# Kernel optimization log

Measured on AMD Instinct MI355X. Metric: run time of the kernel, lower is better.

## Reference

```python
import jax, jax.numpy as jnp
import numpy as np

B, C, H, W = 16384, 1, 2048, 1
HID = 5


def setup_inputs() -> dict:
    key = jax.random.key(0)
    kx, kl, k1, k2, k3, k4 = jax.random.split(key, 6)
    x = jax.random.normal(kx, (B, C, H, W), dtype=jnp.float32)
    # random ragged lengths in [1, H]; zero out padded tail so the module's
    # (x != 0).any(dim=2) mask recovers exactly these lengths
    lengths = jax.random.randint(kl, (B,), 1, H + 1)
    t_idx = jnp.arange(H)
    valid = (t_idx[None, :] < lengths[:, None])  # [B, H]
    x = x * valid[:, None, :, None].astype(jnp.float32)
    s = 1.0 / np.sqrt(HID)
    W_ih = jax.random.uniform(k1, (4 * HID, 1), minval=-s, maxval=s, dtype=jnp.float32)
    W_hh = jax.random.uniform(k2, (4 * HID, HID), minval=-s, maxval=s, dtype=jnp.float32)
    b_ih = jax.random.uniform(k3, (4 * HID,), minval=-s, maxval=s, dtype=jnp.float32)
    b_hh = jax.random.uniform(k4, (4 * HID,), minval=-s, maxval=s, dtype=jnp.float32)
    return {"x": x, "W_ih": W_ih, "W_hh": W_hh, "b_ih": b_ih, "b_hh": b_hh}


def reference(x, W_ih, W_hh, b_ih, b_hh):
    b, c, h, w = x.shape
    feats = c * w  # == 1 (LSTM input_size)
    xr = x.reshape(b, h, feats)  # [B, T, 1]
    mask = jnp.any(xr != 0, axis=2)  # [B, T]
    lengths = mask.sum(axis=1).astype(jnp.int32)  # [B]

    bias = b_ih + b_hh  # [4H]
    # precompute input projection for all timesteps: [B, T, 4H]
    x_proj = jnp.einsum('btf,gf->btg', xr, W_ih) + bias
    xs = jnp.moveaxis(x_proj, 1, 0)  # [T, B, 4H]

    h0 = jnp.zeros((b, HID), dtype=x.dtype)
    c0 = jnp.zeros((b, HID), dtype=x.dtype)

    def step(carry, inp):
        hp, cp = carry
        xg, t = inp
        gates = xg + hp @ W_hh.T  # [B, 4H]
        i, f, g, o = jnp.split(gates, 4, axis=1)
        i = jax.nn.sigmoid(i)
        f = jax.nn.sigmoid(f)
        g = jnp.tanh(g)
        o = jax.nn.sigmoid(o)
        cn = f * cp + i * g
        hn = o * jnp.tanh(cn)
        # packed semantics: only advance state while t < length (per sample)
        upd = (t < lengths)[:, None]
        hn = jnp.where(upd, hn, hp)
        cn = jnp.where(upd, cn, cp)
        return (hn, cn), None

    (hT, cT), _ = jax.lax.scan(step, (h0, c0), (xs, jnp.arange(h)))
    return hT[None]  # [1, B, HID] matching torch h shape
```

## Files before the change

kernel.cpp:

```cpp
#include <hip/hip_runtime.h>

#define Bn    16384
#define Tn    2048
#define HIDn  5
#define NBINS 2048

typedef float v2f __attribute__((ext_vector_type(2)));

static __device__ __forceinline__ float rcp_fast(float v) {
    return __builtin_amdgcn_rcpf(v);
}
static __device__ __forceinline__ float med3(float x, float lo, float hi) {
    return __builtin_amdgcn_fmed3f(x, lo, hi);
}

template <int K>
static __device__ __forceinline__ float bcast8(float v) {
    return __int_as_float(
        __builtin_amdgcn_ds_swizzle(__float_as_int(v), (K << 5) | 0x18));
}

__global__ void zero_kernel(int* __restrict__ gbins) {
    gbins[blockIdx.x * 256 + threadIdx.x] = 0;
}

__global__ __launch_bounds__(256) void len_kernel(const float* __restrict__ x,
                                                  int* __restrict__ lengths,
                                                  int* __restrict__ gbins) {
    const int gtid = blockIdx.x * 256 + threadIdx.x;
    const int row  = gtid >> 6;
    const int lane = threadIdx.x & 63;
    const float4* r = reinterpret_cast<const float4*>(x + (size_t)row * Tn);
    int cnt = 0;
    #pragma unroll
    for (int i = 0; i < Tn / 4 / 64; ++i) {
        float4 v = r[i * 64 + lane];
        cnt += (v.x != 0.0f) + (v.y != 0.0f) + (v.z != 0.0f) + (v.w != 0.0f);
    }
    #pragma unroll
    for (int off = 32; off > 0; off >>= 1) cnt += __shfl_xor(cnt, off, 64);
    if (lane == 0) {
        lengths[row] = cnt;
        const int d = max(0, min(NBINS - 1, NBINS - cnt));
        atomicAdd(&gbins[d], 1);
    }
}

__global__ __launch_bounds__(1024) void sort_kernel(const int* __restrict__ lengths,
                                                    const int* __restrict__ gbins,
                                                    int* __restrict__ perm) {
    __shared__ int bins[NBINS];
    __shared__ int bsum[1024];
    const int tid = threadIdx.x;
    bins[tid]        = gbins[tid];
    bins[tid + 1024] = gbins[tid + 1024];
    __syncthreads();
    const int a0 = bins[2 * tid], a1 = bins[2 * tid + 1];
    const int s = a0 + a1;
    bsum[tid] = s;
    __syncthreads();
    int acc = s;
    for (int off = 1; off < 1024; off <<= 1) {
        int v = (tid >= off) ? bsum[tid - off] : 0;
        __syncthreads();
        acc += v;
        bsum[tid] = acc;
        __syncthreads();
    }
    const int excl = acc - s;
    bins[2 * tid]     = excl;
    bins[2 * tid + 1] = excl + a0;
    __syncthreads();
    for (int i = tid; i < Bn; i += 1024) {
        int d = NBINS - lengths[i];
        d = max(0, min(NBINS - 1, d));
        const int p = atomicAdd(&bins[d], 1);
        perm[p] = i;
    }
}

__global__ __launch_bounds__(256, 2) void lstm_kernel(const float* __restrict__ x,
                                                      const float* __restrict__ Wih,
                                                      const float* __restrict__ Whh,
                                                      const float* __restrict__ bih,
                                                      const float* __restrict__ bhh,
                                                      const int* __restrict__ lengths,
                                                      const int* __restrict__ perm,
                                                      float* __restrict__ out) {
    const int gtid = blockIdx.x * 256 + threadIdx.x;
    const int grp  = gtid >> 3;
    const int lsub = threadIdx.x & 7;
    const int k    = min(lsub, 4);

    const int b   = perm[grp];
    const int len = lengths[b];

    v2f wihA, wihB, bA, bB, whhA[HIDn], whhB[HIDn];
    {
        const int gi = k, gf = 5 + k, gg = 10 + k, go = 15 + k;
        wihA = (v2f){ Wih[gi] * 0.5f, Wih[gf] * 0.5f };
        wihB = (v2f){ Wih[gg],        Wih[go] * 0.5f };
        bA   = (v2f){ (bih[gi] + bhh[gi]) * 0.5f, (bih[gf] + bhh[gf]) * 0.5f };
        bB   = (v2f){ (bih[gg] + bhh[gg]),        (bih[go] + bhh[go]) * 0.5f };
        #pragma unroll
        for (int kk = 0; kk < HIDn; ++kk) {
            whhA[kk] = (v2f){ Whh[gi * HIDn + kk] * 0.5f, Whh[gf * HIDn + kk] * 0.5f };
            whhB[kk] = (v2f){ Whh[gg * HIDn + kk],        Whh[go * HIDn + kk] * 0.5f };
        }
    }

    const float* xrow = x + (size_t)b * Tn;
    float h0 = 0, h1 = 0, h2 = 0, h3 = 0, h4 = 0;
    float hq = 0, c = 0;

    float4 xq = *reinterpret_cast<const float4*>(xrow);
    for (int t = 0; __any(t < len); t += 4) {
        const float4 xn = *reinterpret_cast<const float4*>(xrow + min(t + 4, Tn - 4));
        const float xs[4] = { xq.x, xq.y, xq.z, xq.w };
        #pragma unroll
        for (int s = 0; s < 4; ++s) {
            const float xv = xs[s];
            v2f pA = xv * wihA + bA;
            v2f pB = xv * wihB + bB;
            pA = h0 * whhA[0] + pA;  pB = h0 * whhB[0] + pB;
            pA = h1 * whhA[1] + pA;  pB = h1 * whhB[1] + pB;
            pA = h2 * whhA[2] + pA;  pB = h2 * whhB[2] + pB;
            pA = h3 * whhA[3] + pA;  pB = h3 * whhB[3] + pB;
            pA = h4 * whhA[4] + pA;  pB = h4 * whhB[4] + pB;
            v2f tA, tB;
            tA.x = med3(pA.x, -4.0f, 4.0f);  tA.y = med3(pA.y, -4.0f, 4.0f);
            tB.x = med3(pB.x, -4.0f, 4.0f);  tB.y = med3(pB.y, -4.0f, 4.0f);
            const v2f zA = tA * tA, zB = tB * tB;
            const v2f nA = (zA * 21.0f + 1260.0f) * zA + 10395.0f;
            const v2f nB = (zB * 21.0f + 1260.0f) * zB + 10395.0f;
            const v2f dA = ((zA + 210.0f) * zA + 4725.0f) * zA + 10395.0f;
            const v2f dB = ((zB + 210.0f) * zB + 4725.0f) * zB + 10395.0f;
            const float rA = rcp_fast(dA.x * dA.y);
            const float rB = rcp_fast(dB.x * dB.y);
            const v2f pnA = tA * nA, pnB = tB * nB;
            const float ti = (pnA.x * dA.y) * rA;
            const float tf = (pnA.y * dA.x) * rA;
            const float tg = (pnB.x * dB.y) * rB;
            const float to = (pnB.y * dB.x) * rB;
            const float gi_ = fmaf(ti, 0.5f, 0.5f);
            const float gf_ = fmaf(tf, 0.5f, 0.5f);
            const float oo  = fmaf(to, 0.5f, 0.5f);

            const float cn = fmaf(gf_, c, gi_ * tg);

            const float tc = med3(cn, -4.0f, 4.0f);
            const float zc = tc * tc;
            const float nc = fmaf(zc, fmaf(zc, 21.0f, 1260.0f), 10395.0f);
            const float dc = fmaf(zc, fmaf(zc, zc + 210.0f, 4725.0f), 10395.0f);
            const float hn = (tc * nc) * (oo * rcp_fast(dc));

            const bool upd = (t + s) < len;
            c  = upd ? cn : c;
            hq = upd ? hn : hq;

            h0 = bcast8<0>(hq);
            h1 = bcast8<1>(hq);
            h2 = bcast8<2>(hq);
            h3 = bcast8<3>(hq);
            h4 = bcast8<4>(hq);
        }
        xq = xn;
    }

    if (lsub < HIDn) out[(size_t)b * HIDn + lsub] = hq;
}

extern "C" void kernel_launch(void* const* d_in, const int* in_sizes, int n_in,
                              void* d_out, int out_size, void* d_ws, size_t ws_size,
                              hipStream_t stream) {
    const float* x   = (const float*)d_in[0];
    const float* Wih = (const float*)d_in[1];
    const float* Whh = (const float*)d_in[2];
    const float* bih = (const float*)d_in[3];
    const float* bhh = (const float*)d_in[4];
    float* out = (float*)d_out;

    int* lengths = (int*)d_ws;
    int* perm    = lengths + Bn;
    int* gbins   = perm + Bn;

    zero_kernel<<<NBINS / 256, 256, 0, stream>>>(gbins);
    len_kernel<<<Bn / 4, 256, 0, stream>>>(x, lengths, gbins);
    sort_kernel<<<1, 1024, 0, stream>>>(lengths, gbins, perm);
    lstm_kernel<<<Bn * 8 / 256, 256, 0, stream>>>(x, Wih, Whh, bih, bhh,
                                                  lengths, perm, out);
}
```

Before: 572.9 us.

## Interleave two independent LSTM sequences per 8-lane group for ILP

Each 8-lane group now advances two sorted-adjacent sequences in lockstep, interleaving their per-step gate math and swizzle broadcasts so the two independent dependency chains can hide each other's latency. The grid is halved and the launch bound drops to one block per SIMD to allow the extra registers. The gate scaling is also partly packed into v2f ops. The costs are fewer resident waves and running each pair to the longer of the two lengths.

```diff
diff --git a/kernel.cpp b/kernel.cpp
--- a/kernel.cpp
+++ b/kernel.cpp
@@ -79,7 +79,51 @@
     }
 }
 
-__global__ __launch_bounds__(256, 2) void lstm_kernel(const float* __restrict__ x,
+static __device__ __forceinline__ void lstm_step(
+    float xv, bool upd,
+    v2f wihA, v2f wihB, v2f bA, v2f bB,
+    const v2f* __restrict__ whhA, const v2f* __restrict__ whhB,
+    float h0, float h1, float h2, float h3, float h4,
+    float& hq, float& c)
+{
+    v2f pA = xv * wihA + bA;
+    v2f pB = xv * wihB + bB;
+    pA = h0 * whhA[0] + pA;  pB = h0 * whhB[0] + pB;
+    pA = h1 * whhA[1] + pA;  pB = h1 * whhB[1] + pB;
+    pA = h2 * whhA[2] + pA;  pB = h2 * whhB[2] + pB;
+    pA = h3 * whhA[3] + pA;  pB = h3 * whhB[3] + pB;
+    pA = h4 * whhA[4] + pA;  pB = h4 * whhB[4] + pB;
+    v2f tA, tB;
+    tA.x = med3(pA.x, -4.0f, 4.0f);  tA.y = med3(pA.y, -4.0f, 4.0f);
+    tB.x = med3(pB.x, -4.0f, 4.0f);  tB.y = med3(pB.y, -4.0f, 4.0f);
+    const v2f zA = tA * tA, zB = tB * tB;
+    const v2f nA = (zA * 21.0f + 1260.0f) * zA + 10395.0f;
+    const v2f nB = (zB * 21.0f + 1260.0f) * zB + 10395.0f;
+    const v2f dA = ((zA + 210.0f) * zA + 4725.0f) * zA + 10395.0f;
+    const v2f dB = ((zB + 210.0f) * zB + 4725.0f) * zB + 10395.0f;
+    const float rA = rcp_fast(dA.x * dA.y);
+    const float rB = rcp_fast(dB.x * dB.y);
+    const v2f pnA = tA * nA, pnB = tB * nB;
+    const v2f dAs = {dA.y, dA.x};
+    const v2f dBs = {dB.y, dB.x};
+    const v2f tAv = (pnA * dAs) * rA;
+    const v2f tBv = (pnB * dBs) * rB;
+    const v2f sA = tAv * 0.5f + 0.5f;
+    const v2f sB = tBv * (v2f){1.0f, 0.5f} + (v2f){0.0f, 0.5f};
+
+    const float cn = fmaf(sA.y, c, sA.x * sB.x);
+
+    const float tc = med3(cn, -4.0f, 4.0f);
+    const float zc = tc * tc;
+    const float nc = fmaf(zc, fmaf(zc, 21.0f, 1260.0f), 10395.0f);
+    const float dc = fmaf(zc, fmaf(zc, zc + 210.0f, 4725.0f), 10395.0f);
+    const float hn = (tc * nc) * (sB.y * rcp_fast(dc));
+
+    c  = upd ? cn : c;
+    hq = upd ? hn : hq;
+}
+
+__global__ __launch_bounds__(256, 1) void lstm_kernel(const float* __restrict__ x,
                                                       const float* __restrict__ Wih,
                                                       const float* __restrict__ Whh,
                                                       const float* __restrict__ bih,
@@ -92,8 +136,11 @@
     const int lsub = threadIdx.x & 7;
     const int k    = min(lsub, 4);
 
-    const int b   = perm[grp];
-    const int len = lengths[b];
+    const int ra = perm[2 * grp];
+    const int rb = perm[2 * grp + 1];
+    const int lenA = lengths[ra];
+    const int lenB = lengths[rb];
+    const int lenM = max(lenA, lenB);
 
     v2f wihA, wihB, bA, bB, whhA[HIDn], whhB[HIDn];
     {
@@ -109,65 +156,47 @@
         }
     }
 
-    const float* xrow = x + (size_t)b * Tn;
-    float h0 = 0, h1 = 0, h2 = 0, h3 = 0, h4 = 0;
-    float hq = 0, c = 0;
-
-    float4 xq = *reinterpret_cast<const float4*>(xrow);
-    for (int t = 0; __any(t < len); t += 4) {
-        const float4 xn = *reinterpret_cast<const float4*>(xrow + min(t + 4, Tn - 4));
-        const float xs[4] = { xq.x, xq.y, xq.z, xq.w };
+    const float* xrA = x + (size_t)ra * Tn;
+    const float* xrB = x + (size_t)rb * Tn;
+
+    float hA0 = 0, hA1 = 0, hA2 = 0, hA3 = 0, hA4 = 0, hqA = 0, cA = 0;
+    float hB0 = 0, hB1 = 0, hB2 = 0, hB3 = 0, hB4 = 0, hqB = 0, cB = 0;
+
+    float4 xqA = *reinterpret_cast<const float4*>(xrA);
+    float4 xqB = *reinterpret_cast<const float4*>(xrB);
+
+    for (int t = 0; __any(t < lenM); t += 4) {
+        const int tn = min(t + 4, Tn - 4);
+        const float4 xnA = *reinterpret_cast<const float4*>(xrA + tn);
+        const float4 xnB = *reinterpret_cast<const float4*>(xrB + tn);
+        const float xsA[4] = { xqA.x, xqA.y, xqA.z, xqA.w };
+        const float xsB[4] = { xqB.x, xqB.y, xqB.z, xqB.w };
         #pragma unroll
         for (int s = 0; s < 4; ++s) {
-            const float xv = xs[s];
-            v2f pA = xv * wihA + bA;
-            v2f pB = xv * wihB + bB;
-            pA = h0 * whhA[0] + pA;  pB = h0 * whhB[0] + pB;
-            pA = h1 * whhA[1] + pA;  pB = h1 * whhB[1] + pB;
-            pA = h2 * whhA[2] + pA;  pB = h2 * whhB[2] + pB;
-            pA = h3 * whhA[3] + pA;  pB = h3 * whhB[3] + pB;
-            pA = h4 * whhA[4] + pA;  pB = h4 * whhB[4] + pB;
-            v2f tA, tB;
-            tA.x = med3(pA.x, -4.0f, 4.0f);  tA.y = med3(pA.y, -4.0f, 4.0f);
-            tB.x = med3(pB.x, -4.0f, 4.0f);  tB.y = med3(pB.y, -4.0f, 4.0f);
-            const v2f zA = tA * tA, zB = tB * tB;
-            const v2f nA = (zA * 21.0f + 1260.0f) * zA + 10395.0f;
-            const v2f nB = (zB * 21.0f + 1260.0f) * zB + 10395.0f;
-            const v2f dA = ((zA + 210.0f) * zA + 4725.0f) * zA + 10395.0f;
-            const v2f dB = ((zB + 210.0f) * zB + 4725.0f) * zB + 10395.0f;
-            const float rA = rcp_fast(dA.x * dA.y);
-            const float rB = rcp_fast(dB.x * dB.y);
-            const v2f pnA = tA * nA, pnB = tB * nB;
-            const float ti = (pnA.x * dA.y) * rA;
-            const float tf = (pnA.y * dA.x) * rA;
-            const float tg = (pnB.x * dB.y) * rB;
-            const float to = (pnB.y * dB.x) * rB;
-            const float gi_ = fmaf(ti, 0.5f, 0.5f);
-            const float gf_ = fmaf(tf, 0.5f, 0.5f);
-            const float oo  = fmaf(to, 0.5f, 0.5f);
-
-            const float cn = fmaf(gf_, c, gi_ * tg);
-
-            const float tc = med3(cn, -4.0f, 4.0f);
-            const float zc = tc * tc;
-            const float nc = fmaf(zc, fmaf(zc, 21.0f, 1260.0f), 10395.0f);
-            const float dc = fmaf(zc, fmaf(zc, zc + 210.0f, 4725.0f), 10395.0f);
-            const float hn = (tc * nc) * (oo * rcp_fast(dc));
-
-            const bool upd = (t + s) < len;
-            c  = upd ? cn : c;
-            hq = upd ? hn : hq;
-
-            h0 = bcast8<0>(hq);
-            h1 = bcast8<1>(hq);
-            h2 = bcast8<2>(hq);
-            h3 = bcast8<3>(hq);
-            h4 = bcast8<4>(hq);
+            lstm_step(xsA[s], (t + s) < lenA, wihA, wihB, bA, bB, whhA, whhB,
+                      hA0, hA1, hA2, hA3, hA4, hqA, cA);
+            hA0 = bcast8<0>(hqA);
+            hA1 = bcast8<1>(hqA);
+            hA2 = bcast8<2>(hqA);
+            hA3 = bcast8<3>(hqA);
+            hA4 = bcast8<4>(hqA);
+
+            lstm_step(xsB[s], (t + s) < lenB, wihA, wihB, bA, bB, whhA, whhB,
+                      hB0, hB1, hB2, hB3, hB4, hqB, cB);
+            hB0 = bcast8<0>(hqB);
+            hB1 = bcast8<1>(hqB);
+            hB2 = bcast8<2>(hqB);
+            hB3 = bcast8<3>(hqB);
+            hB4 = bcast8<4>(hqB);
         }
-        xq = xn;
-    }
-
-    if (lsub < HIDn) out[(size_t)b * HIDn + lsub] = hq;
+        xqA = xnA;
+        xqB = xnB;
+    }
+
+    if (lsub < HIDn) {
+        out[(size_t)ra * HIDn + lsub] = hqA;
+        out[(size_t)rb * HIDn + lsub] = hqB;
+    }
 }
 
 extern "C" void kernel_launch(void* const* d_in, const int* in_sizes, int n_in,
@@ -187,6 +216,6 @@
     zero_kernel<<<NBINS / 256, 256, 0, stream>>>(gbins);
     len_kernel<<<Bn / 4, 256, 0, stream>>>(x, lengths, gbins);
     sort_kernel<<<1, 1024, 0, stream>>>(lengths, gbins, perm);
-    lstm_kernel<<<Bn * 8 / 256, 256, 0, stream>>>(x, Wih, Whh, bih, bhh,
+    lstm_kernel<<<Bn * 8 / 512, 256, 0, stream>>>(x, Wih, Whh, bih, bhh,
                                                   lengths, perm, out);
 }
```

Result: slower. 809.0 us (+41.2%).

## Map each LSTM sample to four lanes with DPP quad broadcast of hidden state

Applied to the files above, without the earlier changes.

Each sample now uses 4 lanes instead of 8. Every lane computes two hidden units: its own unit k, plus unit 4 computed redundantly by all four lanes. The hidden-state exchange moves from ds_swizzle to quad DPP moves, which do not go through the LDS path, and unit 4 is read locally. This halves the thread count and removes the 3 idle lanes per group. In exchange each lane does roughly double the arithmetic, uses more registers, and the occupancy hint drops to 1.

```diff
diff --git a/kernel.cpp b/kernel.cpp
--- a/kernel.cpp
+++ b/kernel.cpp
@@ -15,9 +15,10 @@
 }
 
 template <int K>
-static __device__ __forceinline__ float bcast8(float v) {
+static __device__ __forceinline__ float qbcast(float v) {
+    constexpr int ctrl = K | (K << 2) | (K << 4) | (K << 6);
     return __int_as_float(
-        __builtin_amdgcn_ds_swizzle(__float_as_int(v), (K << 5) | 0x18));
+        __builtin_amdgcn_mov_dpp(__float_as_int(v), ctrl, 0xF, 0xF, true));
 }
 
 __global__ void zero_kernel(int* __restrict__ gbins) {
@@ -79,7 +80,7 @@
     }
 }
 
-__global__ __launch_bounds__(256, 2) void lstm_kernel(const float* __restrict__ x,
+__global__ __launch_bounds__(256, 1) void lstm_kernel(const float* __restrict__ x,
                                                       const float* __restrict__ Wih,
                                                       const float* __restrict__ Whh,
                                                       const float* __restrict__ bih,
@@ -88,30 +89,37 @@
                                                       const int* __restrict__ perm,
                                                       float* __restrict__ out) {
     const int gtid = blockIdx.x * 256 + threadIdx.x;
-    const int grp  = gtid >> 3;
-    const int lsub = threadIdx.x & 7;
-    const int k    = min(lsub, 4);
+    const int grp  = gtid >> 2;
+    const int k    = threadIdx.x & 3;
 
     const int b   = perm[grp];
     const int len = lengths[b];
 
-    v2f wihA, wihB, bA, bB, whhA[HIDn], whhB[HIDn];
-    {
-        const int gi = k, gf = 5 + k, gg = 10 + k, go = 15 + k;
-        wihA = (v2f){ Wih[gi] * 0.5f, Wih[gf] * 0.5f };
-        wihB = (v2f){ Wih[gg],        Wih[go] * 0.5f };
-        bA   = (v2f){ (bih[gi] + bhh[gi]) * 0.5f, (bih[gf] + bhh[gf]) * 0.5f };
-        bB   = (v2f){ (bih[gg] + bhh[gg]),        (bih[go] + bhh[go]) * 0.5f };
-        #pragma unroll
-        for (int kk = 0; kk < HIDn; ++kk) {
-            whhA[kk] = (v2f){ Whh[gi * HIDn + kk] * 0.5f, Whh[gf * HIDn + kk] * 0.5f };
-            whhB[kk] = (v2f){ Whh[gg * HIDn + kk],        Whh[go * HIDn + kk] * 0.5f };
-        }
+    const int ri0 = k,      ri1 = 4;
+    const int rf0 = 5 + k,  rf1 = 9;
+    const int rg0 = 10 + k, rg1 = 14;
+    const int ro0 = 15 + k, ro1 = 19;
+
+    const v2f wI = { Wih[ri0] * 0.5f, Wih[ri1] * 0.5f };
+    const v2f wF = { Wih[rf0] * 0.5f, Wih[rf1] * 0.5f };
+    const v2f wG = { Wih[rg0],        Wih[rg1]        };
+    const v2f wO = { Wih[ro0] * 0.5f, Wih[ro1] * 0.5f };
+    const v2f bI = { (bih[ri0] + bhh[ri0]) * 0.5f, (bih[ri1] + bhh[ri1]) * 0.5f };
+    const v2f bF = { (bih[rf0] + bhh[rf0]) * 0.5f, (bih[rf1] + bhh[rf1]) * 0.5f };
+    const v2f bG = { (bih[rg0] + bhh[rg0]),        (bih[rg1] + bhh[rg1])        };
+    const v2f bO = { (bih[ro0] + bhh[ro0]) * 0.5f, (bih[ro1] + bhh[ro1]) * 0.5f };
+    v2f hI[HIDn], hF[HIDn], hG[HIDn], hO[HIDn];
+    #pragma unroll
+    for (int j = 0; j < HIDn; ++j) {
+        hI[j] = (v2f){ Whh[ri0 * HIDn + j] * 0.5f, Whh[ri1 * HIDn + j] * 0.5f };
+        hF[j] = (v2f){ Whh[rf0 * HIDn + j] * 0.5f, Whh[rf1 * HIDn + j] * 0.5f };
+        hG[j] = (v2f){ Whh[rg0 * HIDn + j],        Whh[rg1 * HIDn + j]        };
+        hO[j] = (v2f){ Whh[ro0 * HIDn + j] * 0.5f, Whh[ro1 * HIDn + j] * 0.5f };
     }
 
     const float* xrow = x + (size_t)b * Tn;
+    v2f hq = { 0.0f, 0.0f }, c = { 0.0f, 0.0f };
     float h0 = 0, h1 = 0, h2 = 0, h3 = 0, h4 = 0;
-    float hq = 0, c = 0;
 
     float4 xq = *reinterpret_cast<const float4*>(xrow);
     for (int t = 0; __any(t < len); t += 4) {
@@ -120,54 +128,66 @@
         #pragma unroll
         for (int s = 0; s < 4; ++s) {
             const float xv = xs[s];
-            v2f pA = xv * wihA + bA;
-            v2f pB = xv * wihB + bB;
-            pA = h0 * whhA[0] + pA;  pB = h0 * whhB[0] + pB;
-            pA = h1 * whhA[1] + pA;  pB = h1 * whhB[1] + pB;
-            pA = h2 * whhA[2] + pA;  pB = h2 * whhB[2] + pB;
-            pA = h3 * whhA[3] + pA;  pB = h3 * whhB[3] + pB;
-            pA = h4 * whhA[4] + pA;  pB = h4 * whhB[4] + pB;
-            v2f tA, tB;
-            tA.x = med3(pA.x, -4.0f, 4.0f);  tA.y = med3(pA.y, -4.0f, 4.0f);
-            tB.x = med3(pB.x, -4.0f, 4.0f);  tB.y = med3(pB.y, -4.0f, 4.0f);
-            const v2f zA = tA * tA, zB = tB * tB;
-            const v2f nA = (zA * 21.0f + 1260.0f) * zA + 10395.0f;
-            const v2f nB = (zB * 21.0f + 1260.0f) * zB + 10395.0f;
-            const v2f dA = ((zA + 210.0f) * zA + 4725.0f) * zA + 10395.0f;
-            const v2f dB = ((zB + 210.0f) * zB + 4725.0f) * zB + 10395.0f;
-            const float rA = rcp_fast(dA.x * dA.y);
-            const float rB = rcp_fast(dB.x * dB.y);
-            const v2f pnA = tA * nA, pnB = tB * nB;
-            const float ti = (pnA.x * dA.y) * rA;
-            const float tf = (pnA.y * dA.x) * rA;
-            const float tg = (pnB.x * dB.y) * rB;
-            const float to = (pnB.y * dB.x) * rB;
-            const float gi_ = fmaf(ti, 0.5f, 0.5f);
-            const float gf_ = fmaf(tf, 0.5f, 0.5f);
-            const float oo  = fmaf(to, 0.5f, 0.5f);
-
-            const float cn = fmaf(gf_, c, gi_ * tg);
-
-            const float tc = med3(cn, -4.0f, 4.0f);
-            const float zc = tc * tc;
-            const float nc = fmaf(zc, fmaf(zc, 21.0f, 1260.0f), 10395.0f);
-            const float dc = fmaf(zc, fmaf(zc, zc + 210.0f, 4725.0f), 10395.0f);
-            const float hn = (tc * nc) * (oo * rcp_fast(dc));
+            v2f pI = xv * wI + bI;
+            v2f pF = xv * wF + bF;
+            v2f pG = xv * wG + bG;
+            v2f pO = xv * wO + bO;
+            pI = h0 * hI[0] + pI; pF = h0 * hF[0] + pF; pG = h0 * hG[0] + pG; pO = h0 * hO[0] + pO;
+            pI = h1 * hI[1] + pI; pF = h1 * hF[1] + pF; pG = h1 * hG[1] + pG; pO = h1 * hO[1] + pO;
+            pI = h2 * hI[2] + pI; pF = h2 * hF[2] + pF; pG = h2 * hG[2] + pG; pO = h2 * hO[2] + pO;
+            pI = h3 * hI[3] + pI; pF = h3 * hF[3] + pF; pG = h3 * hG[3] + pG; pO = h3 * hO[3] + pO;
+            pI = h4 * hI[4] + pI; pF = h4 * hF[4] + pF; pG = h4 * hG[4] + pG; pO = h4 * hO[4] + pO;
+            v2f tI, tF, tG, tO;
+            tI.x = med3(pI.x, -4.0f, 4.0f);  tI.y = med3(pI.y, -4.0f, 4.0f);
+            tF.x = med3(pF.x, -4.0f, 4.0f);  tF.y = med3(pF.y, -4.0f, 4.0f);
+            tG.x = med3(pG.x, -4.0f, 4.0f);  tG.y = med3(pG.y, -4.0f, 4.0f);
+            tO.x = med3(pO.x, -4.0f, 4.0f);  tO.y = med3(pO.y, -4.0f, 4.0f);
+            const v2f zI = tI * tI, zF = tF * tF, zG = tG * tG, zO = tO * tO;
+            const v2f nI = (zI * 21.0f + 1260.0f) * zI + 10395.0f;
+            const v2f nF = (zF * 21.0f + 1260.0f) * zF + 10395.0f;
+            const v2f nG = (zG * 21.0f + 1260.0f) * zG + 10395.0f;
+            const v2f nO = (zO * 21.0f + 1260.0f) * zO + 10395.0f;
+            const v2f dI = ((zI + 210.0f) * zI + 4725.0f) * zI + 10395.0f;
+            const v2f dF = ((zF + 210.0f) * zF + 4725.0f) * zF + 10395.0f;
+            const v2f dG = ((zG + 210.0f) * zG + 4725.0f) * zG + 10395.0f;
+            const v2f dO = ((zO + 210.0f) * zO + 4725.0f) * zO + 10395.0f;
+            const v2f prIF = dI * dF;
+            const v2f prGO = dG * dO;
+            const v2f rIF = { rcp_fast(prIF.x), rcp_fast(prIF.y) };
+            const v2f rGO = { rcp_fast(prGO.x), rcp_fast(prGO.y) };
+            const v2f thI = ((tI * nI) * dF) * rIF;
+            const v2f thF = ((tF * nF) * dI) * rIF;
+            const v2f thG = ((tG * nG) * dO) * rGO;
+            const v2f thO = ((tO * nO) * dG) * rGO;
+            const v2f sI = thI * 0.5f + 0.5f;
+            const v2f sF = thF * 0.5f + 0.5f;
+            const v2f sO = thO * 0.5f + 0.5f;
+
+            const v2f cn = sF * c + sI * thG;
+
+            v2f tc;
+            tc.x = med3(cn.x, -4.0f, 4.0f);  tc.y = med3(cn.y, -4.0f, 4.0f);
+            const v2f zc = tc * tc;
+            const v2f nc = (zc * 21.0f + 1260.0f) * zc + 10395.0f;
+            const v2f dc = ((zc + 210.0f) * zc + 4725.0f) * zc + 10395.0f;
+            const v2f rc = { rcp_fast(dc.x), rcp_fast(dc.y) };
+            const v2f hn = (tc * nc) * (sO * rc);
 
             const bool upd = (t + s) < len;
-            c  = upd ? cn : c;
-            hq = upd ? hn : hq;
-
-            h0 = bcast8<0>(hq);
-            h1 = bcast8<1>(hq);
-            h2 = bcast8<2>(hq);
-            h3 = bcast8<3>(hq);
-            h4 = bcast8<4>(hq);
+            c.x  = upd ? cn.x : c.x;    c.y  = upd ? cn.y : c.y;
+            hq.x = upd ? hn.x : hq.x;   hq.y = upd ? hn.y : hq.y;
+
+            h0 = qbcast<0>(hq.x);
+            h1 = qbcast<1>(hq.x);
+            h2 = qbcast<2>(hq.x);
+            h3 = qbcast<3>(hq.x);
+            h4 = hq.y;
         }
         xq = xn;
     }
 
-    if (lsub < HIDn) out[(size_t)b * HIDn + lsub] = hq;
+    out[(size_t)b * HIDn + k] = hq.x;
+    if (k == 3) out[(size_t)b * HIDn + 4] = hq.y;
 }
 
 extern "C" void kernel_launch(void* const* d_in, const int* in_sizes, int n_in,
@@ -187,6 +207,6 @@
     zero_kernel<<<NBINS / 256, 256, 0, stream>>>(gbins);
     len_kernel<<<Bn / 4, 256, 0, stream>>>(x, lengths, gbins);
     sort_kernel<<<1, 1024, 0, stream>>>(lengths, gbins, perm);
-    lstm_kernel<<<Bn * 8 / 256, 256, 0, stream>>>(x, Wih, Whh, bih, bhh,
+    lstm_kernel<<<Bn * 4 / 256, 256, 0, stream>>>(x, Wih, Whh, bih, bhh,
                                                   lengths, perm, out);
 }
```

New measurement: 703.7 us. 1.23x slower.
